# Performance work log

Hardware: AMD Instinct MI355X
Metric: run time of the kernel (lower is better)

## Reference

```python
import jax, jax.numpy as jnp
import numpy as np

SIGMA = 0.3
EPS = 1e-8  # torch CosineSimilarity eps
LOG_SQRT_2PI = float(0.5 * np.log(2.0 * np.pi))


def setup_inputs() -> dict:
    key = jax.random.key(0)
    k1, k2 = jax.random.split(key)
    Ex = jax.random.normal(k1, (8192, 256), dtype=jnp.float32)
    Ey = jax.random.normal(k2, (8192, 256), dtype=jnp.float32)
    return {"Ex": Ex, "Ey": Ey}


def reference(Ex, Ey):
    # cosine similarity: normalize rows (clamped norms), then dot -> [n, m]
    xn = Ex / jnp.maximum(jnp.linalg.norm(Ex, axis=-1, keepdims=True), EPS)
    yn = Ey / jnp.maximum(jnp.linalg.norm(Ey, axis=-1, keepdims=True), EPS)
    M = jnp.einsum('nd,md->nm', xn, yn)
    # Normal(loc=1, scale=sigma).log_prob
    z = (M - 1.0) / SIGMA
    logp = -0.5 * z * z - jnp.log(jnp.asarray(SIGMA, M.dtype)) - LOG_SQRT_2PI
    # C = -(exp(logp) * logp); row-wise min over y-tokens -> [n]
    C = -jnp.exp(logp) * logp
    return jnp.min(C, axis=-1)
```

## Files before the change

kernel.cpp:

```cpp
#include <hip/hip_runtime.h>
#include <hip/hip_bf16.h>

typedef unsigned short u16;
typedef __attribute__((ext_vector_type(8))) short short8;
typedef __attribute__((ext_vector_type(4))) float floatx4;

#define NROWS 8192
#define DIM 256

__device__ __forceinline__ void atomicMinFloat(float* addr, float val) {
    if (val >= 0.0f) {
        atomicMin((int*)addr, __float_as_int(val));
    } else {
        atomicMax((unsigned int*)addr, __float_as_uint(val));
    }
}

__device__ __forceinline__ u16 f32_to_bf16_rne(float x) {
    unsigned int u = __float_as_uint(x);
    unsigned int r = (u + 0x7fffu + ((u >> 16) & 1u)) >> 16;
    return (u16)r;
}

__device__ __forceinline__ float c_of_m(float m) {
    const float INV_SIG = 1.0f / 0.3f;
    const float KC = 0.28503427f;
    float z = (m - 1.0f) * INV_SIG;
    float logp = fmaf(-0.5f * z, z, KC);
    return -logp * __expf(logp);
}

__device__ __forceinline__ void load16(const u16* g, u16* l) {
    __builtin_amdgcn_global_load_lds(
        (__attribute__((address_space(1))) void*)g,
        (__attribute__((address_space(3))) void*)l, 16, 0, 0);
}

__global__ __launch_bounds__(256) void normalize_kernel(const float* __restrict__ Ex,
                                                        const float* __restrict__ Ey,
                                                        u16* __restrict__ Xs,
                                                        u16* __restrict__ Ys,
                                                        float* __restrict__ out) {
    const int t = threadIdx.x;
    const int ln = t & 63;
    const int row = blockIdx.x * 4 + (t >> 6);
    const float* src = (blockIdx.y == 0) ? Ex : Ey;
    u16* dst = (blockIdx.y == 0) ? Xs : Ys;

    float4 v = *(const float4*)(src + (size_t)row * DIM + ln * 4);
    float s = fmaf(v.x, v.x, fmaf(v.y, v.y, fmaf(v.z, v.z, v.w * v.w)));
    #pragma unroll
    for (int m = 32; m >= 1; m >>= 1) s += __shfl_xor(s, m, 64);
    float inv = 1.0f / fmaxf(sqrtf(s), 1e-8f);

    ushort4 o;
    o.x = f32_to_bf16_rne(v.x * inv);
    o.y = f32_to_bf16_rne(v.y * inv);
    o.z = f32_to_bf16_rne(v.z * inv);
    o.w = f32_to_bf16_rne(v.w * inv);

    const int p = row >> 4;
    const int lm = row & 15;
    const int kt = ln >> 3;
    const int lq = (ln >> 1) & 3;
    const int j4 = (ln & 1) * 4;
    const size_t off = ((size_t)((p * 8 + kt) * 64 + lq * 16 + lm)) * 8 + j4;
    *(ushort4*)(dst + off) = o;

    if (blockIdx.y == 0 && ln == 0) out[row] = __uint_as_float(0x7f800000u);
}

__global__ void __launch_bounds__(512, 2)
gemm_min_kernel(const u16* __restrict__ Xs,
                const u16* __restrict__ Ys,
                float* __restrict__ out) {
    __shared__ u16 Bs[2][16 * 512];

    const int tid = threadIdx.x;
    const int w = tid >> 6;
    const int lane = tid & 63;
    const int lq = lane >> 4;
    const int lm = lane & 15;

    const int i = blockIdx.x;
    const int x = i & 7;
    const int jj = i >> 3;
    const int rt = (x & 3) * 4 + (jj & 3);
    const int cgrp = (x >> 2) * 8 + (jj >> 2);

    const int rowStart = rt * 512;
    const int rowPan0 = rt * 32 + w * 4;
    const u16* ybase = Ys + (size_t)cgrp * 32 * 4096;

    auto stage1 = [&](int buf, const u16* yb, int iu) {
        const int u = w * 2 + iu;
        load16(yb + (u >> 3) * 4096 + (u & 7) * 512 + lane * 8,
               &Bs[buf][u * 512]);
    };

    short8 a[4][8];
    auto loadA = [&](int kt) {
        #pragma unroll
        for (int rg = 0; rg < 4; ++rg)
            a[rg][kt] = *(const short8*)(
                Xs + ((size_t)(rowPan0 + rg) * 8 + kt) * 512 + lane * 8);
    };

    floatx4 mn4[4], mx4[4];
    #pragma unroll
    for (int rg = 0; rg < 4; ++rg) {
        mn4[rg] = (floatx4){3.4e38f, 3.4e38f, 3.4e38f, 3.4e38f};
        mx4[rg] = (floatx4){-3.4e38f, -3.4e38f, -3.4e38f, -3.4e38f};
    }

    floatx4 acc[4][2];
    const floatx4 FZ = (floatx4){0.0f, 0.0f, 0.0f, 0.0f};

    auto fold = [&]() {
        #pragma unroll
        for (int rg = 0; rg < 4; ++rg)
            #pragma unroll
            for (int cg = 0; cg < 2; ++cg)
                #pragma unroll
                for (int r = 0; r < 4; ++r) {
                    float m = acc[rg][cg][r];
                    mn4[rg][r] = fminf(mn4[rg][r], m);
                    mx4[rg][r] = fmaxf(mx4[rg][r], m);
                }
    };

    auto compute = [&](int buf, int dofold) {
        const u16* bsb = &Bs[buf][0];
        short8 bfA[2], bfB[2];
        #pragma unroll
        for (int cg = 0; cg < 2; ++cg)
            bfA[cg] = *(const short8*)(bsb + (cg * 8 + 0) * 512 + lane * 8);
        #pragma unroll
        for (int cg = 0; cg < 2; ++cg)
            bfB[cg] = *(const short8*)(bsb + (cg * 8 + 1) * 512 + lane * 8);
        if (dofold) fold();
        #pragma unroll
        for (int k2 = 0; k2 < 4; ++k2) {
            const int ke = 2 * k2;
            const int ko = ke + 1;
            if (ke == 0) {
                #pragma unroll
                for (int cg = 0; cg < 2; ++cg)
                    #pragma unroll
                    for (int rg = 0; rg < 4; ++rg)
                        acc[rg][cg] = __builtin_amdgcn_mfma_f32_16x16x32_bf16(
                            a[rg][0], bfA[cg], FZ, 0, 0, 0);
            } else {
                #pragma unroll
                for (int cg = 0; cg < 2; ++cg)
                    #pragma unroll
                    for (int rg = 0; rg < 4; ++rg)
                        acc[rg][cg] = __builtin_amdgcn_mfma_f32_16x16x32_bf16(
                            a[rg][ke], bfA[cg], acc[rg][cg], 0, 0, 0);
            }
            if (ke + 2 < 8) {
                #pragma unroll
                for (int cg = 0; cg < 2; ++cg)
                    bfA[cg] = *(const short8*)(bsb + (cg * 8 + ke + 2) * 512 + lane * 8);
            }
            #pragma unroll
            for (int cg = 0; cg < 2; ++cg)
                #pragma unroll
                for (int rg = 0; rg < 4; ++rg)
                    acc[rg][cg] = __builtin_amdgcn_mfma_f32_16x16x32_bf16(
                        a[rg][ko], bfB[cg], acc[rg][cg], 0, 0, 0);
            if (ko + 2 < 8) {
                #pragma unroll
                for (int cg = 0; cg < 2; ++cg)
                    bfB[cg] = *(const short8*)(bsb + (cg * 8 + ko + 2) * 512 + lane * 8);
            }
        }
    };

    stage1(0, ybase, 0); stage1(0, ybase, 1);
    loadA(0); loadA(1);
    __syncthreads();
    stage1(1, ybase + 8192, 0); stage1(1, ybase + 8192, 1);
    loadA(2); loadA(3); loadA(4); loadA(5); loadA(6); loadA(7);
    compute(0, 0);
    ybase += 8192;

    #pragma unroll 1
    for (int ct = 1; ct < 16; ++ct) {
        const int buf = ct & 1;
        __syncthreads();
        if (ct < 15)
            stage1(buf ^ 1, ybase + 8192, 0), stage1(buf ^ 1, ybase + 8192, 1);
        compute(buf, 1);
        ybase += 8192;
    }
    fold();

    #pragma unroll
    for (int rg = 0; rg < 4; ++rg) {
        #pragma unroll
        for (int r = 0; r < 4; ++r) {
            float mn = mn4[rg][r];
            float mx = mx4[rg][r];
            #pragma unroll
            for (int mofs = 1; mofs < 16; mofs <<= 1) {
                mn = fminf(mn, __shfl_xor(mn, mofs, 64));
                mx = fmaxf(mx, __shfl_xor(mx, mofs, 64));
            }
            if (lm == 0) {
                float cmin = fminf(c_of_m(mn), c_of_m(mx));
                int row = rowStart + w * 64 + rg * 16 + lq * 4 + r;
                atomicMinFloat(&out[row], cmin);
            }
        }
    }
}

extern "C" void kernel_launch(void* const* d_in, const int* in_sizes, int n_in,
                              void* d_out, int out_size, void* d_ws, size_t ws_size,
                              hipStream_t stream) {
    const float* Ex = (const float*)d_in[0];
    const float* Ey = (const float*)d_in[1];
    float* out = (float*)d_out;
    u16* Xs = (u16*)d_ws;
    u16* Ys = Xs + (size_t)NROWS * DIM;

    hipLaunchKernelGGL(normalize_kernel, dim3(NROWS / 4, 2), dim3(256), 0, stream,
                       Ex, Ey, Xs, Ys, out);
    hipLaunchKernelGGL(gemm_min_kernel, dim3(16 * 16), dim3(512), 0, stream,
                       Xs, Ys, out);
}
```

Baseline: 93.72 us.

## Fuse normalization into GEMM-min kernel via cooperative grid sync

```diff
diff --git a/kernel.cpp b/kernel.cpp
--- a/kernel.cpp
+++ b/kernel.cpp
@@ -1,5 +1,8 @@
 #include <hip/hip_runtime.h>
 #include <hip/hip_bf16.h>
+#include <hip/hip_cooperative_groups.h>
+
+namespace cg = cooperative_groups;
 
 typedef unsigned short u16;
 typedef __attribute__((ext_vector_type(8))) short short8;
@@ -36,49 +39,53 @@
         (__attribute__((address_space(3))) void*)l, 16, 0, 0);
 }
 
-__global__ __launch_bounds__(256) void normalize_kernel(const float* __restrict__ Ex,
-                                                        const float* __restrict__ Ey,
-                                                        u16* __restrict__ Xs,
-                                                        u16* __restrict__ Ys,
-                                                        float* __restrict__ out) {
-    const int t = threadIdx.x;
-    const int ln = t & 63;
-    const int row = blockIdx.x * 4 + (t >> 6);
-    const float* src = (blockIdx.y == 0) ? Ex : Ey;
-    u16* dst = (blockIdx.y == 0) ? Xs : Ys;
-
-    float4 v = *(const float4*)(src + (size_t)row * DIM + ln * 4);
-    float s = fmaf(v.x, v.x, fmaf(v.y, v.y, fmaf(v.z, v.z, v.w * v.w)));
-    #pragma unroll
-    for (int m = 32; m >= 1; m >>= 1) s += __shfl_xor(s, m, 64);
-    float inv = 1.0f / fmaxf(sqrtf(s), 1e-8f);
-
-    ushort4 o;
-    o.x = f32_to_bf16_rne(v.x * inv);
-    o.y = f32_to_bf16_rne(v.y * inv);
-    o.z = f32_to_bf16_rne(v.z * inv);
-    o.w = f32_to_bf16_rne(v.w * inv);
-
-    const int p = row >> 4;
-    const int lm = row & 15;
-    const int kt = ln >> 3;
-    const int lq = (ln >> 1) & 3;
-    const int j4 = (ln & 1) * 4;
-    const size_t off = ((size_t)((p * 8 + kt) * 64 + lq * 16 + lm)) * 8 + j4;
-    *(ushort4*)(dst + off) = o;
-
-    if (blockIdx.y == 0 && ln == 0) out[row] = __uint_as_float(0x7f800000u);
-}
-
 __global__ void __launch_bounds__(512, 2)
-gemm_min_kernel(const u16* __restrict__ Xs,
-                const u16* __restrict__ Ys,
-                float* __restrict__ out) {
+fused_kernel(const float* __restrict__ Ex,
+             const float* __restrict__ Ey,
+             u16* __restrict__ Xs,
+             u16* __restrict__ Ys,
+             float* __restrict__ out) {
     __shared__ u16 Bs[2][16 * 512];
 
     const int tid = threadIdx.x;
     const int w = tid >> 6;
     const int lane = tid & 63;
+
+    {
+        const int gr0 = blockIdx.x * 64 + w * 8;
+        const bool isX = gr0 < NROWS;
+        const float* src = isX ? Ex : Ey;
+        u16* dst = isX ? Xs : Ys;
+        #pragma unroll
+        for (int s = 0; s < 8; ++s) {
+            const int row = (gr0 + s) & (NROWS - 1);
+            float4 v = *(const float4*)(src + (size_t)row * DIM + lane * 4);
+            float sm = fmaf(v.x, v.x, fmaf(v.y, v.y, fmaf(v.z, v.z, v.w * v.w)));
+            #pragma unroll
+            for (int m = 32; m >= 1; m >>= 1) sm += __shfl_xor(sm, m, 64);
+            float inv = 1.0f / fmaxf(sqrtf(sm), 1e-8f);
+
+            ushort4 o;
+            o.x = f32_to_bf16_rne(v.x * inv);
+            o.y = f32_to_bf16_rne(v.y * inv);
+            o.z = f32_to_bf16_rne(v.z * inv);
+            o.w = f32_to_bf16_rne(v.w * inv);
+
+            const int p = row >> 4;
+            const int lmn = row & 15;
+            const int ktn = lane >> 3;
+            const int lqn = (lane >> 1) & 3;
+            const int j4 = (lane & 1) * 4;
+            const size_t off =
+                ((size_t)((p * 8 + ktn) * 64 + lqn * 16 + lmn)) * 8 + j4;
+            *(ushort4*)(dst + off) = o;
+
+            if (isX && lane == 0) out[row] = __uint_as_float(0x7f800000u);
+        }
+    }
+
+    cg::this_grid().sync();
+
     const int lq = lane >> 4;
     const int lm = lane & 15;
 
@@ -225,8 +232,7 @@
     u16* Xs = (u16*)d_ws;
     u16* Ys = Xs + (size_t)NROWS * DIM;
 
-    hipLaunchKernelGGL(normalize_kernel, dim3(NROWS / 4, 2), dim3(256), 0, stream,
-                       Ex, Ey, Xs, Ys, out);
-    hipLaunchKernelGGL(gemm_min_kernel, dim3(16 * 16), dim3(512), 0, stream,
-                       Xs, Ys, out);
-}
+    void* args[] = {(void*)&Ex, (void*)&Ey, (void*)&Xs, (void*)&Ys, (void*)&out};
+    hipLaunchCooperativeKernel((const void*)fused_kernel, dim3(256), dim3(512),
+                               args, 0, stream);
+}
```

Measured after the change: 146.8 us. 56.6% more time.
